# Kernel tuning notes

Measured on AMD Instinct MI355X. Metric: run time of the kernel, lower is better.

The kernel has to match this reference:

```python
import jax, jax.numpy as jnp
import numpy as np

ALPHA = 0.2  # LeakyReLU negative slope
OUT_FEATURES = 64

def setup_inputs() -> dict:
    key = jax.random.key(0)
    k1, k2, k3 = jax.random.split(key, 3)
    B, N, F_in, F_out = 16, 2048, 64, OUT_FEATURES
    h = jax.random.normal(k1, (B, N, F_in), dtype=jnp.float32)
    W = jax.random.normal(k2, (F_in, F_out), dtype=jnp.float32) * (1.414 / np.sqrt(F_in))
    a = jax.random.normal(k3, (2 * F_out, 1), dtype=jnp.float32) * 1.414
    return {"h": h, "W": W, "a": a}

def reference(h, W, a):
    F_out = W.shape[1]
    Wh = jnp.matmul(h, W)                        # [B, N, F_out]
    Wh1 = jnp.matmul(Wh, a[:F_out, :])           # [B, N, 1]
    Wh2 = jnp.matmul(Wh, a[F_out:, :])           # [B, N, 1]
    e = Wh1 + jnp.transpose(Wh2, (0, 2, 1))      # [B, N, N] broadcast add
    e = jnp.where(e >= 0, e, ALPHA * e)          # LeakyReLU
    attention = jax.nn.softmax(jax.nn.sigmoid(e), axis=1)  # softmax over dim=1 (faithful to source)
    h_prime = jnp.matmul(attention, Wh)          # [B, N, F_out]
    return jax.nn.elu(h_prime)                   # concat=True -> ELU
```

## Files before the change

kernel.cpp:

```cpp
#include <hip/hip_runtime.h>
#include <hip/hip_bf16.h>
#include <math.h>

#define NB 16
#define NN 2048
#define NF 64
#define LOG2E 1.44269504f

#define NT 4096
#define T_LO (-40.0f)
#define T_HI (10.0f)
#define T_SCALE (NT / (T_HI - T_LO))
#define Z_BIAS (-T_LO * T_SCALE)
#define Z_MAX ((float)(NT - 1))

#define MG 512
#define XG_LO (-96.0f)
#define DXG 0.375f
#define INV_DXG (1.0f / DXG)
#define U_BIAS (-XG_LO * INV_DXG)
#define U_MAX 510.999f

#define MGG 256
#define DXGG 0.75f
#define UG_MAX 254.999f
#define GS_N 1024

typedef __attribute__((ext_vector_type(8))) __bf16 bf16x8;
typedef __attribute__((ext_vector_type(8))) short  short8;
typedef __attribute__((ext_vector_type(4))) float  f32x4;

__device__ __forceinline__ float gexact(float t) {
    float v = t >= 0.f ? t : 0.2f * t;
    float s = 1.f / (1.f + expf(-v));
    return expf(s);
}

__device__ __forceinline__ float tlookup(const float* __restrict__ stab, float z) {
    float zc = __builtin_amdgcn_fmed3f(z, 0.f, Z_MAX);
    return stab[(int)zc];
}

__device__ __forceinline__ float elu(float v) {
    return v > 0.f ? v : (__builtin_amdgcn_exp2f(v * LOG2E) - 1.f);
}

__global__ __launch_bounds__(256) void k_prep(const float* __restrict__ h,
                                              const float* __restrict__ W,
                                              const float* __restrict__ a,
                                              uint4* __restrict__ vfrag,
                                              float* __restrict__ ys,
                                              float* __restrict__ xs_u,
                                              float* __restrict__ ys_u,
                                              float* __restrict__ Fpart,
                                              float* __restrict__ gtab) {
    __shared__ __attribute__((aligned(16))) float  hT[64 * 68];
    __shared__ __attribute__((aligned(16))) __bf16 WbT[64 * 72];
    __shared__ __attribute__((aligned(16))) __bf16 vT[64 * 74];
    __shared__ float uv[128];
    __shared__ float gsb[GS_N];
    __shared__ int   kuA[64];
    __shared__ float frA[64];
    int t  = threadIdx.x;
    int r0 = blockIdx.x * 64;
    int b  = blockIdx.x >> 5;
#pragma unroll
    for (int i = t; i < GS_N; i += 256)
        gsb[i] = gexact(2.f * XG_LO + (float)i * DXG);
    const float4* hsrc = (const float4*)(h + r0 * 64);
#pragma unroll
    for (int i = 0; i < 4; i++) {
        int flat = t + i * 256;
        int row = flat >> 4, c4 = flat & 15;
        float4 hv = hsrc[flat];
        float* dst = &hT[row * 68 + c4 * 4];
        dst[0] = hv.x; dst[1] = hv.y; dst[2] = hv.z; dst[3] = hv.w;
    }
#pragma unroll
    for (int i = 0; i < 4; i++) {
        int flat = t + i * 256;
        int k = flat >> 4, c4 = flat & 15;
        float4 wv = ((const float4*)W)[flat];
        WbT[(c4 * 4 + 0) * 72 + k] = (__bf16)wv.x;
        WbT[(c4 * 4 + 1) * 72 + k] = (__bf16)wv.y;
        WbT[(c4 * 4 + 2) * 72 + k] = (__bf16)wv.z;
        WbT[(c4 * 4 + 3) * 72 + k] = (__bf16)wv.w;
    }
    if (t < 64) {
        float s = 0.f;
#pragma unroll 8
        for (int f = 0; f < 64; f++) s = fmaf(W[t * 64 + f], a[f], s);
        uv[t] = s;
    } else if (t < 128) {
        int k = t - 64;
        float s = 0.f;
#pragma unroll 8
        for (int f = 0; f < 64; f++) s = fmaf(W[k * 64 + f], a[64 + f], s);
        uv[64 + k] = s;
    }
    __syncthreads();
    {
        int row = t >> 2, q = t & 3;
        const float* hp = &hT[row * 68 + q * 16];
        const float* up = &uv[q * 16];
        const float* vp = &uv[64 + q * 16];
        float sx = 0.f, sy = 0.f;
#pragma unroll
        for (int k2 = 0; k2 < 16; k2++) {
            float hv = hp[k2];
            sx = fmaf(hv, up[k2], sx);
            sy = fmaf(hv, vp[k2], sy);
        }
        sx += __shfl_xor(sx, 1); sx += __shfl_xor(sx, 2);
        sy += __shfl_xor(sy, 1); sy += __shfl_xor(sy, 2);
        if (q == 0) {
            int r = r0 + row;
            float xu = __builtin_amdgcn_fmed3f(sx * INV_DXG + U_BIAS, 0.f, U_MAX);
            ys[r]   = T_SCALE * sy;
            xs_u[r] = xu;
            ys_u[r] = __builtin_amdgcn_fmed3f(sy * INV_DXG + U_BIAS, 0.f, U_MAX);
            int ku  = (int)xu;
            kuA[row] = ku;
            frA[row] = xu - (float)ku;
        }
    }
    int w = t >> 6, lane = t & 63;
    int il = lane & 15, kg = lane >> 4;
    f32x4 acc0 = {0.f,0.f,0.f,0.f}, acc1 = {0.f,0.f,0.f,0.f};
    f32x4 acc2 = {0.f,0.f,0.f,0.f}, acc3 = {0.f,0.f,0.f,0.f};
#pragma unroll
    for (int ks = 0; ks < 2; ks++) {
        const float* ap = &hT[(w * 16 + il) * 68 + ks * 32 + kg * 8];
        bf16x8 af;
#pragma unroll
        for (int e = 0; e < 8; e++) af[e] = (__bf16)ap[e];
        bf16x8 b0 = *(const bf16x8*)&WbT[(0 * 16 + il) * 72 + ks * 32 + kg * 8];
        bf16x8 b1 = *(const bf16x8*)&WbT[(1 * 16 + il) * 72 + ks * 32 + kg * 8];
        bf16x8 b2 = *(const bf16x8*)&WbT[(2 * 16 + il) * 72 + ks * 32 + kg * 8];
        bf16x8 b3 = *(const bf16x8*)&WbT[(3 * 16 + il) * 72 + ks * 32 + kg * 8];
        acc0 = __builtin_amdgcn_mfma_f32_16x16x32_bf16(af, b0, acc0, 0, 0, 0);
        acc1 = __builtin_amdgcn_mfma_f32_16x16x32_bf16(af, b1, acc1, 0, 0, 0);
        acc2 = __builtin_amdgcn_mfma_f32_16x16x32_bf16(af, b2, acc2, 0, 0, 0);
        acc3 = __builtin_amdgcn_mfma_f32_16x16x32_bf16(af, b3, acc3, 0, 0, 0);
    }
#pragma unroll
    for (int r = 0; r < 4; r++) {
        __bf16* vrow = &vT[(w * 16 + kg * 4 + r) * 74 + il];
        vrow[0]  = (__bf16)acc0[r];
        vrow[16] = (__bf16)acc1[r];
        vrow[32] = (__bf16)acc2[r];
        vrow[48] = (__bf16)acc3[r];
    }
    __syncthreads();
#pragma unroll
    for (int s = 0; s < 2; s++) {
        int oi    = t + s * 256;
        int lane2 = oi & 63;
        int nt2   = (oi >> 6) & 3;
        int ksl   = oi >> 8;
        int rbase = ksl * 32 + ((lane2 >> 4) << 3);
        int col   = nt2 * 16 + (lane2 & 15);
        short8 o;
#pragma unroll
        for (int e = 0; e < 8; e++)
            o[e] = __builtin_bit_cast(short, vT[(rbase + e) * 74 + col]);
        int ks_g = ((blockIdx.x & 31) << 1) | ksl;
        vfrag[((b * 64 + ks_g) * 4 + nt2) * 64 + lane2] = __builtin_bit_cast(uint4, o);
    }
    {
        float a0 = 0.f, a1 = 0.f;
#pragma unroll 8
        for (int r = 0; r < 64; r++) {
            int   ku = kuA[r];
            float fr = frA[r];
            float w0 = 1.f - fr;
            const float* g0 = &gsb[ku + t];
            const float* g1 = &gsb[ku + t + 256];
            a0 = fmaf(w0, g0[0], a0); a0 = fmaf(fr, g0[1], a0);
            a1 = fmaf(w0, g1[0], a1); a1 = fmaf(fr, g1[1], a1);
        }
        Fpart[blockIdx.x * MG + t]       = a0;
        Fpart[blockIdx.x * MG + t + 256] = a1;
    }
    if (blockIdx.x < 16) {
        int i = blockIdx.x * 256 + t;
        gtab[i] = gexact(T_LO + ((float)i + 0.5f) / T_SCALE);
    }
}

__global__ __launch_bounds__(512) void k_gbuild(const float* __restrict__ ys,
                                                const float* __restrict__ ys_u,
                                                const float* __restrict__ Fpart,
                                                const float* __restrict__ gtab,
                                                const uint4* __restrict__ vfrag,
                                                float* __restrict__ G) {
    __shared__ float stab[NT];
    __shared__ float dinvb[NN];
    __shared__ float red[7][16][65];
    float* Fb = &red[0][0][0];
    int t = threadIdx.x;
    int b  = blockIdx.x >> 4;
    int ib = blockIdx.x & 15;
    {
        const float4* src = (const float4*)gtab;
        float4*       dst = (float4*)stab;
#pragma unroll
        for (int k = 0; k < NT / 4 / 512; k++) dst[t + k * 512] = src[t + k * 512];
    }
    {
        const float* fp = Fpart + (b * 32) * MG + t;
        float s = 0.f;
#pragma unroll 8
        for (int p = 0; p < 32; p++) s += fp[p * MG];
        Fb[t] = s;
    }
    __syncthreads();
#pragma unroll
    for (int i = 0; i < 4; i++) {
        int j = t + i * 512;
        float u  = ys_u[b * NN + j];
        int   k  = (int)u;
        float fr = u - (float)k;
        float d  = fmaf(Fb[k + 1] - Fb[k], fr, Fb[k]);
        dinvb[j] = __builtin_amdgcn_rcpf(d);
    }
    int kz = t >> 6, lane = t & 63;
    int il = lane & 15, kg = lane >> 4;
    int mbase = ib * 16;

    float xgb = (XG_LO + (float)(mbase + il) * DXGG) * T_SCALE + Z_BIAS;
    const float* ysb = ys + b * NN;
    const uint4* vfb = vfrag + b * 16384 + lane;
    __syncthreads();

    f32x4 acc0 = {0.f,0.f,0.f,0.f}, acc1 = {0.f,0.f,0.f,0.f};
    f32x4 acc2 = {0.f,0.f,0.f,0.f}, acc3 = {0.f,0.f,0.f,0.f};

    for (int ks = kz * 8; ks < kz * 8 + 8; ks++) {
        const float* yp = ysb + ks * 32 + kg * 8;
        const float* dp = &dinvb[ks * 32 + kg * 8];
        float4 ya = *reinterpret_cast<const float4*>(yp);
        float4 yb = *reinterpret_cast<const float4*>(yp + 4);
        float wv[8];
        wv[0] = tlookup(stab, xgb + ya.x);
        wv[1] = tlookup(stab, xgb + ya.y);
        wv[2] = tlookup(stab, xgb + ya.z);
        wv[3] = tlookup(stab, xgb + ya.w);
        wv[4] = tlookup(stab, xgb + yb.x);
        wv[5] = tlookup(stab, xgb + yb.y);
        wv[6] = tlookup(stab, xgb + yb.z);
        wv[7] = tlookup(stab, xgb + yb.w);
        bf16x8 af;
#pragma unroll
        for (int e = 0; e < 8; e++) af[e] = (__bf16)(wv[e] * dp[e]);

        const uint4* vp = vfb + ks * 256;
        bf16x8 b0 = __builtin_bit_cast(bf16x8, vp[0]);
        bf16x8 b1 = __builtin_bit_cast(bf16x8, vp[64]);
        bf16x8 b2 = __builtin_bit_cast(bf16x8, vp[128]);
        bf16x8 b3 = __builtin_bit_cast(bf16x8, vp[192]);

        acc0 = __builtin_amdgcn_mfma_f32_16x16x32_bf16(af, b0, acc0, 0, 0, 0);
        acc1 = __builtin_amdgcn_mfma_f32_16x16x32_bf16(af, b1, acc1, 0, 0, 0);
        acc2 = __builtin_amdgcn_mfma_f32_16x16x32_bf16(af, b2, acc2, 0, 0, 0);
        acc3 = __builtin_amdgcn_mfma_f32_16x16x32_bf16(af, b3, acc3, 0, 0, 0);
    }

    if (kz > 0) {
#pragma unroll
        for (int r = 0; r < 4; r++) {
            float* rp = &red[kz - 1][kg * 4 + r][il];
            rp[0]  = acc0[r];
            rp[16] = acc1[r];
            rp[32] = acc2[r];
            rp[48] = acc3[r];
        }
    }
    __syncthreads();
    if (kz == 0) {
        int gbase = (b * MGG + mbase + kg * 4) * 64 + il;
#pragma unroll
        for (int r = 0; r < 4; r++) {
            float s0 = acc0[r], s1 = acc1[r], s2 = acc2[r], s3 = acc3[r];
#pragma unroll
            for (int p = 0; p < 7; p++) {
                const float* rp = &red[p][kg * 4 + r][il];
                s0 += rp[0]; s1 += rp[16]; s2 += rp[32]; s3 += rp[48];
            }
            float* grow = G + gbase + r * 64;
            grow[0] = s0; grow[16] = s1; grow[32] = s2; grow[48] = s3;
        }
    }
}

__global__ __launch_bounds__(256) void k_apply(const float* __restrict__ xs_u,
                                               const float* __restrict__ G,
                                               float* __restrict__ out) {
    int t   = threadIdx.x;
    int row = blockIdx.x * 16 + (t >> 4);
    int c4  = t & 15;
    int b   = row >> 11;
    float u  = fminf(xs_u[row] * 0.5f, UG_MAX);
    int   k  = (int)u;
    float fr = u - (float)k;
    const float4* Gb = (const float4*)(G + (b * MGG + k) * 64);
    float4 g0 = Gb[c4];
    float4 g1 = Gb[16 + c4];
    float4 r;
    r.x = elu(fmaf(g1.x - g0.x, fr, g0.x));
    r.y = elu(fmaf(g1.y - g0.y, fr, g0.y));
    r.z = elu(fmaf(g1.z - g0.z, fr, g0.z));
    r.w = elu(fmaf(g1.w - g0.w, fr, g0.w));
    reinterpret_cast<float4*>(out)[row * 16 + c4] = r;
}

extern "C" void kernel_launch(void* const* d_in, const int* in_sizes, int n_in,
                              void* d_out, int out_size, void* d_ws, size_t ws_size,
                              hipStream_t stream) {
    const float* h = (const float*)d_in[0];
    const float* W = (const float*)d_in[1];
    const float* a = (const float*)d_in[2];
    float* out = (float*)d_out;

    float*  ys    = (float*)d_ws;
    float*  xs_u  = ys + NB * NN;
    float*  ys_u  = xs_u + NB * NN;
    float*  Fpart = ys_u + NB * NN;
    float*  G     = Fpart + (NB * NN / 64) * MG;
    uint4*  vfrag = (uint4*)(G + NB * MGG * NF);
    float*  gtab  = (float*)(vfrag + NB * NN * NF / 8);

    k_prep<<<dim3(NB * NN / 64), dim3(256), 0, stream>>>(h, W, a, vfrag, ys, xs_u, ys_u, Fpart, gtab);
    k_gbuild<<<dim3(NB * (MGG / 16)), dim3(512), 0, stream>>>(ys, ys_u, Fpart, gtab, vfrag, G);
    k_apply<<<dim3(NB * NN / 16), dim3(256), 0, stream>>>(xs_u, G, out);
}
```

Baseline: 31.12 us.

## Fuse apply stage into gbuild using overlapping 15-row G tiles in LDS

Removes the separate k_apply launch and the global G buffer by having each gbuild block keep its 16 grid rows in shared memory. Tiles now overlap by one row (stride 15, 17 tiles per batch) so that interpolation between neighbouring grid points stays inside one block. Each block scans all rows of its batch, builds a list of rows whose grid index falls in its range via a shared atomic counter, then interpolates, applies ELU and writes the output. This saves a launch and a global round trip, but adds 17/16 more MFMA work, a per-block scan of xs_u and a data-dependent write pattern.

```diff
diff --git a/kernel.cpp b/kernel.cpp
--- a/kernel.cpp
+++ b/kernel.cpp
@@ -25,6 +25,7 @@
 #define DXGG 0.75f
 #define UG_MAX 254.999f
 #define GS_N 1024
+#define TILES 17
 
 typedef __attribute__((ext_vector_type(8))) __bf16 bf16x8;
 typedef __attribute__((ext_vector_type(8))) short  short8;
@@ -190,17 +191,21 @@
 
 __global__ __launch_bounds__(512) void k_gbuild(const float* __restrict__ ys,
                                                 const float* __restrict__ ys_u,
+                                                const float* __restrict__ xs_u,
                                                 const float* __restrict__ Fpart,
                                                 const float* __restrict__ gtab,
                                                 const uint4* __restrict__ vfrag,
-                                                float* __restrict__ G) {
+                                                float* __restrict__ out) {
     __shared__ float stab[NT];
     __shared__ float dinvb[NN];
     __shared__ float red[7][16][65];
+    __shared__ __attribute__((aligned(16))) float Gl[16][64];
+    __shared__ int cnt;
     float* Fb = &red[0][0][0];
     int t = threadIdx.x;
-    int b  = blockIdx.x >> 4;
-    int ib = blockIdx.x & 15;
+    int b  = blockIdx.x / TILES;
+    int ib = blockIdx.x % TILES;
+    int mbase = ib * 15;
     {
         const float4* src = (const float4*)gtab;
         float4*       dst = (float4*)stab;
@@ -226,7 +231,6 @@
     }
     int kz = t >> 6, lane = t & 63;
     int il = lane & 15, kg = lane >> 4;
-    int mbase = ib * 16;
 
     float xgb = (XG_LO + (float)(mbase + il) * DXGG) * T_SCALE + Z_BIAS;
     const float* ysb = ys + b * NN;
@@ -276,9 +280,9 @@
             rp[48] = acc3[r];
         }
     }
+    if (t == 0) cnt = 0;
     __syncthreads();
     if (kz == 0) {
-        int gbase = (b * MGG + mbase + kg * 4) * 64 + il;
 #pragma unroll
         for (int r = 0; r < 4; r++) {
             float s0 = acc0[r], s1 = acc1[r], s2 = acc2[r], s3 = acc3[r];
@@ -287,31 +291,44 @@
                 const float* rp = &red[p][kg * 4 + r][il];
                 s0 += rp[0]; s1 += rp[16]; s2 += rp[32]; s3 += rp[48];
             }
-            float* grow = G + gbase + r * 64;
+            float* grow = &Gl[kg * 4 + r][il];
             grow[0] = s0; grow[16] = s1; grow[32] = s2; grow[48] = s3;
         }
     }
-}
-
-__global__ __launch_bounds__(256) void k_apply(const float* __restrict__ xs_u,
-                                               const float* __restrict__ G,
-                                               float* __restrict__ out) {
-    int t   = threadIdx.x;
-    int row = blockIdx.x * 16 + (t >> 4);
-    int c4  = t & 15;
-    int b   = row >> 11;
-    float u  = fminf(xs_u[row] * 0.5f, UG_MAX);
-    int   k  = (int)u;
-    float fr = u - (float)k;
-    const float4* Gb = (const float4*)(G + (b * MGG + k) * 64);
-    float4 g0 = Gb[c4];
-    float4 g1 = Gb[16 + c4];
-    float4 r;
-    r.x = elu(fmaf(g1.x - g0.x, fr, g0.x));
-    r.y = elu(fmaf(g1.y - g0.y, fr, g0.y));
-    r.z = elu(fmaf(g1.z - g0.z, fr, g0.z));
-    r.w = elu(fmaf(g1.w - g0.w, fr, g0.w));
-    reinterpret_cast<float4*>(out)[row * 16 + c4] = r;
+    __syncthreads();
+    int* rowlist = (int*)&red[0][0][0];
+#pragma unroll
+    for (int i = 0; i < 4; i++) {
+        int row = t + i * 512;
+        float u = fminf(xs_u[b * NN + row] * 0.5f, UG_MAX);
+        int kg2 = (int)u;
+        if (kg2 >= mbase && kg2 <= mbase + 14) {
+            int slot = atomicAdd(&cnt, 1);
+            rowlist[slot] = row;
+        }
+    }
+    __syncthreads();
+    int nrows = cnt;
+    int rl = t >> 4, c4 = t & 15;
+    const float4* Gl4 = (const float4*)&Gl[0][0];
+    for (int base = 0; base < nrows; base += 32) {
+        int idx = base + rl;
+        if (idx < nrows) {
+            int row = rowlist[idx];
+            float u  = fminf(xs_u[b * NN + row] * 0.5f, UG_MAX);
+            int   k  = (int)u;
+            float fr = u - (float)k;
+            int   lk = k - mbase;
+            float4 g0 = Gl4[lk * 16 + c4];
+            float4 g1 = Gl4[(lk + 1) * 16 + c4];
+            float4 r;
+            r.x = elu(fmaf(g1.x - g0.x, fr, g0.x));
+            r.y = elu(fmaf(g1.y - g0.y, fr, g0.y));
+            r.z = elu(fmaf(g1.z - g0.z, fr, g0.z));
+            r.w = elu(fmaf(g1.w - g0.w, fr, g0.w));
+            reinterpret_cast<float4*>(out)[(b * NN + row) * 16 + c4] = r;
+        }
+    }
 }
 
 extern "C" void kernel_launch(void* const* d_in, const int* in_sizes, int n_in,
@@ -326,11 +343,9 @@
     float*  xs_u  = ys + NB * NN;
     float*  ys_u  = xs_u + NB * NN;
     float*  Fpart = ys_u + NB * NN;
-    float*  G     = Fpart + (NB * NN / 64) * MG;
-    uint4*  vfrag = (uint4*)(G + NB * MGG * NF);
+    uint4*  vfrag = (uint4*)(Fpart + (NB * NN / 64) * MG);
     float*  gtab  = (float*)(vfrag + NB * NN * NF / 8);
 
     k_prep<<<dim3(NB * NN / 64), dim3(256), 0, stream>>>(h, W, a, vfrag, ys, xs_u, ys_u, Fpart, gtab);
-    k_gbuild<<<dim3(NB * (MGG / 16)), dim3(512), 0, stream>>>(ys, ys_u, Fpart, gtab, vfrag, G);
-    k_apply<<<dim3(NB * NN / 16), dim3(256), 0, stream>>>(xs_u, G, out);
-}
+    k_gbuild<<<dim3(NB * TILES), dim3(512), 0, stream>>>(ys, ys_u, xs_u, Fpart, gtab, vfrag, out);
+}
```

Result: slower. 37.08 us (+19.1%).
